# Kernel tuning notes

Measured on AMD Instinct MI355X. Metric: run time of the kernel, lower is better.

The kernel has to match this reference:

```python
import jax, jax.numpy as jnp
import numpy as np

EPS = 1e-5

def setup_inputs() -> dict:
    key = jax.random.key(0)
    ks = jax.random.split(key, 5)
    B, T, D = 2, 4096, 512
    x = jax.random.normal(ks[0], (B, T, D), dtype=jnp.float32)
    w_qkv = jax.random.normal(ks[1], (D, 3 * D), dtype=jnp.float32) * (1.0 / np.sqrt(D))
    w_out = jax.random.normal(ks[2], (D, D), dtype=jnp.float32) * (1.0 / np.sqrt(D))
    b_out = jnp.zeros((D,), dtype=jnp.float32)
    gamma = jnp.ones((D,), dtype=jnp.float32)
    beta = jnp.zeros((D,), dtype=jnp.float32)
    return {"x": x, "w_qkv": w_qkv, "w_out": w_out, "b_out": b_out,
            "gamma": gamma, "beta": beta}

def reference(x, w_qkv, w_out, b_out, gamma, beta):
    B, T, D = x.shape
    H = 8
    hd = D // H
    scale = 1.0 / jnp.sqrt(jnp.asarray(hd, x.dtype))
    residual = x
    # pre-norm LayerNorm
    mu = jnp.mean(x, axis=-1, keepdims=True)
    var = jnp.mean((x - mu) ** 2, axis=-1, keepdims=True)
    xn = (x - mu) / jnp.sqrt(var + EPS) * gamma + beta
    # qkv projection (no bias)
    qkv = (xn @ w_qkv).reshape(B, T, 3, H, hd)
    q, k, v = qkv[:, :, 0], qkv[:, :, 1], qkv[:, :, 2]  # (B,T,H,hd)
    # (B,H,T,T) scores with causal mask
    attn = jnp.einsum('bthd,bshd->bhts', q, k) * scale
    causal = jnp.triu(jnp.ones((T, T), dtype=bool), k=1)
    attn = jnp.where(causal[None, None], -jnp.inf, attn)
    attn = jax.nn.softmax(attn, axis=-1)
    out = jnp.einsum('bhts,bshd->bthd', attn, v).reshape(B, T, D)
    out = out @ w_out + b_out
    return out + residual
```

## Files before the change

### kernel.cpp

```cpp
#include <hip/hip_runtime.h>

typedef __attribute__((ext_vector_type(8))) short bh8;
typedef __attribute__((ext_vector_type(4))) float f32x4;
typedef unsigned short u16;

#define MFMA16 __builtin_amdgcn_mfma_f32_16x16x32_bf16

#if __has_builtin(__builtin_amdgcn_exp2f)
#define EXP2(x) __builtin_amdgcn_exp2f(x)
#else
#define EXP2(x) exp2f(x)
#endif

#define CEXP 0.18033688011112042f
#define MBIAS (10.0f * CEXP)

__device__ __forceinline__ u16 f2bf(float f) {
  union { float f; unsigned u; } v; v.f = f;
  unsigned r = v.u + 0x7fffu + ((v.u >> 16) & 1u);
  return (u16)(r >> 16);
}

__device__ __forceinline__ unsigned cvtpk(float lo, float hi) {
  unsigned r;
  asm("v_cvt_pk_bf16_f32 %0, %1, %2" : "=v"(r) : "v"(lo), "v"(hi));
  return r;
}

__device__ __forceinline__ void gload16(void* lds, const void* g) {
  __builtin_amdgcn_global_load_lds(
      (const __attribute__((address_space(1))) unsigned int*)g,
      (__attribute__((address_space(3))) unsigned int*)lds, 16, 0, 0);
}

__global__ __launch_bounds__(256) void k_ln(const float* __restrict__ x,
                                            const float* __restrict__ gamma,
                                            const float* __restrict__ beta,
                                            u16* __restrict__ xn) {
  int row  = blockIdx.x * 4 + (threadIdx.x >> 6);
  int lane = threadIdx.x & 63;
  const float4* xr = (const float4*)(x + row * 512);
  float4 a = xr[lane * 2], b = xr[lane * 2 + 1];
  float s  = a.x + a.y + a.z + a.w + b.x + b.y + b.z + b.w;
  float ss = a.x*a.x + a.y*a.y + a.z*a.z + a.w*a.w
           + b.x*b.x + b.y*b.y + b.z*b.z + b.w*b.w;
#pragma unroll
  for (int m = 1; m < 64; m <<= 1) { s += __shfl_xor(s, m, 64); ss += __shfl_xor(ss, m, 64); }
  float mu  = s * (1.0f / 512.0f);
  float var = ss * (1.0f / 512.0f) - mu * mu;
  float rstd = rsqrtf(var + 1e-5f);
  const float4* g4 = (const float4*)gamma;
  const float4* b4 = (const float4*)beta;
  float4 g0 = g4[lane * 2], g1 = g4[lane * 2 + 1];
  float4 e0 = b4[lane * 2], e1 = b4[lane * 2 + 1];
  bh8 ov;
  ov[0] = (short)f2bf((a.x - mu) * rstd * g0.x + e0.x);
  ov[1] = (short)f2bf((a.y - mu) * rstd * g0.y + e0.y);
  ov[2] = (short)f2bf((a.z - mu) * rstd * g0.z + e0.z);
  ov[3] = (short)f2bf((a.w - mu) * rstd * g0.w + e0.w);
  ov[4] = (short)f2bf((b.x - mu) * rstd * g1.x + e1.x);
  ov[5] = (short)f2bf((b.y - mu) * rstd * g1.y + e1.y);
  ov[6] = (short)f2bf((b.z - mu) * rstd * g1.z + e1.z);
  ov[7] = (short)f2bf((b.w - mu) * rstd * g1.w + e1.w);
  *(bh8*)(xn + row * 512 + lane * 8) = ov;
}

__global__ __launch_bounds__(256) void k_transpose_cast(const float* __restrict__ in,
                                                        u16* __restrict__ out,
                                                        int R, int C) {
  __shared__ float tile[32][33];
  int c0 = blockIdx.x * 32, r0 = blockIdx.y * 32;
  int tx = threadIdx.x & 31, ty = threadIdx.x >> 5;
#pragma unroll
  for (int i = 0; i < 32; i += 8)
    tile[ty + i][tx] = in[(r0 + ty + i) * C + (c0 + tx)];
  __syncthreads();
#pragma unroll
  for (int i = 0; i < 32; i += 8)
    out[(c0 + ty + i) * R + (r0 + tx)] = f2bf(tile[tx][ty + i]);
}

template <int EPI>
__global__ __launch_bounds__(256) void k_gemm(const u16* __restrict__ A,
                                              const u16* __restrict__ Bt,
                                              int N,
                                              u16* __restrict__ q, u16* __restrict__ kk, u16* __restrict__ vt,
                                              const float* __restrict__ bias,
                                              const float* __restrict__ resid,
                                              float* __restrict__ outp) {
  constexpr int K = 512, BM = 128, BK = 64;
  __shared__ u16 Al[BM * BK];
  __shared__ u16 Bl[BM * BK];
  int nBN = N / 128;
  int bid = (blockIdx.x & 7) * (gridDim.x >> 3) + (blockIdx.x >> 3);
  int m0 = (bid / nBN) * BM;
  int n0 = (bid % nBN) * 128;
  int tid = threadIdx.x, lane = tid & 63, w = tid >> 6;
  int l16 = lane & 15, lh = lane >> 4;
  int wm = (w >> 1) * 64, wn = (w & 1) * 64;
  const u16* Ab = A + m0 * K;
  const u16* Bb = Bt + n0 * K;
  f32x4 acc[4][4];
#pragma unroll
  for (int i = 0; i < 4; ++i)
#pragma unroll
    for (int j = 0; j < 4; ++j) acc[i][j] = (f32x4){0.f, 0.f, 0.f, 0.f};
  int srow = tid >> 3, schunk = tid & 7;
  for (int k0 = 0; k0 < K; k0 += BK) {
    __syncthreads();
#pragma unroll
    for (int j = 0; j < 4; ++j) {
      int r = j * 32 + srow;
      int sc = ((schunk ^ (r & 7)) << 3);
      gload16((char*)Al + j * 4096 + tid * 16, Ab + r * K + k0 + sc);
      gload16((char*)Bl + j * 4096 + tid * 16, Bb + r * K + k0 + sc);
    }
    __syncthreads();
#pragma unroll
    for (int c = 0; c < 2; ++c) {
      bh8 af[4], bf[4];
#pragma unroll
      for (int i = 0; i < 4; ++i) {
        int ra = wm + i * 16 + l16;
        af[i] = *(const bh8*)&Al[ra * 64 + ((c * 32 + lh * 8) ^ ((ra & 7) << 3))];
        int rb = wn + i * 16 + l16;
        bf[i] = *(const bh8*)&Bl[rb * 64 + ((c * 32 + lh * 8) ^ ((rb & 7) << 3))];
      }
#pragma unroll
      for (int mi = 0; mi < 4; ++mi)
#pragma unroll
        for (int ni = 0; ni < 4; ++ni)
          acc[mi][ni] = MFMA16(af[mi], bf[ni], acc[mi][ni], 0, 0, 0);
    }
  }
  if (EPI == 0) {
#pragma unroll
    for (int mi = 0; mi < 4; ++mi)
#pragma unroll
      for (int ni = 0; ni < 4; ++ni) {
        int col = n0 + wn + ni * 16 + l16;
        int s = col >> 9, h = (col >> 6) & 7, d = col & 63;
        int row0 = m0 + wm + mi * 16 + lh * 4;
        int b = row0 >> 12, t0 = row0 & 4095;
        if (s == 2) {
          uint2 pk;
          pk.x = cvtpk(acc[mi][ni][0], acc[mi][ni][1]);
          pk.y = cvtpk(acc[mi][ni][2], acc[mi][ni][3]);
          *(uint2*)&vt[((size_t)((b << 3) + h) * 64 + d) * 4096 + t0] = pk;
        } else {
          u16* base = (s == 0 ? q : kk);
#pragma unroll
          for (int j = 0; j < 4; ++j)
            base[(((size_t)(b << 3) + h) * 4096 + t0 + j) * 64 + d] = f2bf(acc[mi][ni][j]);
        }
      }
  } else {
#pragma unroll
    for (int mi = 0; mi < 4; ++mi)
#pragma unroll
      for (int ni = 0; ni < 4; ++ni) {
        int col = n0 + wn + ni * 16 + l16;
        float bo = bias[col];
#pragma unroll
        for (int j = 0; j < 4; ++j) {
          int row = m0 + wm + mi * 16 + lh * 4 + j;
          outp[row * 512 + col] = acc[mi][ni][j] + bo + resid[row * 512 + col];
        }
      }
  }
}

__global__ __launch_bounds__(256) void k_attn(const u16* __restrict__ Q,
                                              const u16* __restrict__ Kg,
                                              const u16* __restrict__ Vt,
                                              u16* __restrict__ O) {
  __shared__ u16 Kl[2 * 64 * 64];
  __shared__ u16 Vl[2 * 64 * 64];
  __shared__ u16 Pl[4 * 1024];
  int bh = blockIdx.x & 15;
  int qi = 63 - (blockIdx.x >> 4);
  int tid = threadIdx.x, lane = tid & 63, w = tid >> 6;
  int l16 = lane & 15, lh = lane >> 4;
  const u16* Qb = Q + bh * 4096 * 64;
  const u16* Kb = Kg + bh * 4096 * 64;
  const u16* Vb = Vt + (size_t)bh * 64 * 4096;
  int q0 = qi * 64;
  int myq = q0 + w * 16 + l16;
  bh8 qf0 = *(const bh8*)(Qb + myq * 64 + lh * 8);
  bh8 qf1 = *(const bh8*)(Qb + myq * 64 + 32 + lh * 8);
  float l_ = 0.f;
  f32x4 acc[4];
#pragma unroll
  for (int dn = 0; dn < 4; ++dn) acc[dn] = (f32x4){0.f, 0.f, 0.f, 0.f};
  int srow = tid >> 3, schunk = tid & 7;
  u16* pw = Pl + w * 1024 + l16 * 64;
  int pswz = (l16 & 7) << 3;

  for (int kt = 0; kt <= qi; kt += 2) {
    __syncthreads();
#pragma unroll
    for (int t = 0; t < 2; ++t) {
      int kk = (kt + t) * 64;
#pragma unroll
      for (int j = 0; j < 2; ++j) {
        int r = j * 32 + srow;
        int sc = ((schunk ^ (r & 7)) << 3);
        gload16((char*)Kl + t * 8192 + j * 4096 + tid * 16, Kb + (kk + r) * 64 + sc);
        gload16((char*)Vl + t * 8192 + j * 4096 + tid * 16, Vb + r * 4096 + kk + sc);
      }
    }
    __syncthreads();
    int k0 = kt * 64;
    f32x4 s[8];
    __builtin_amdgcn_s_setprio(1);
#pragma unroll
    for (int g = 0; g < 8; ++g) {
      const u16* Kc = Kl + (g >> 2) * 4096;
      int r = (g & 3) * 16 + l16;
      bh8 kf0 = *(const bh8*)&Kc[r * 64 + ((lh * 8) ^ ((r & 7) << 3))];
      bh8 kf1 = *(const bh8*)&Kc[r * 64 + ((32 + lh * 8) ^ ((r & 7) << 3))];
      f32x4 z = (f32x4){0.f, 0.f, 0.f, 0.f};
      z = MFMA16(kf0, qf0, z, 0, 0, 0);
      z = MFMA16(kf1, qf1, z, 0, 0, 0);
      s[g] = z;
    }
    __builtin_amdgcn_s_setprio(0);
    if (kt + 2 > qi) {
#pragma unroll
      for (int g = 0; g < 8; ++g)
#pragma unroll
        for (int j = 0; j < 4; ++j) {
          int tk = k0 + g * 16 + lh * 4 + j;
          if (tk > myq) s[g][j] = -3e38f;
        }
    }
#pragma unroll
    for (int g = 0; g < 8; ++g) {
      float p0 = EXP2(fmaf(s[g][0], CEXP, -MBIAS));
      float p1 = EXP2(fmaf(s[g][1], CEXP, -MBIAS));
      float p2 = EXP2(fmaf(s[g][2], CEXP, -MBIAS));
      float p3 = EXP2(fmaf(s[g][3], CEXP, -MBIAS));
      l_ += (p0 + p1) + (p2 + p3);
      s[g][0] = p0; s[g][1] = p1; s[g][2] = p2; s[g][3] = p3;
    }
#pragma unroll
    for (int h = 0; h < 2; ++h) {
#pragma unroll
      for (int f = 0; f < 4; ++f) {
        int g = h * 4 + f;
        uint2 pk;
        pk.x = cvtpk(s[g][0], s[g][1]);
        pk.y = cvtpk(s[g][2], s[g][3]);
        *(uint2*)&pw[(f * 16 + lh * 4) ^ pswz] = pk;
      }
      bh8 pa0 = *(const bh8*)&pw[(lh * 8) ^ pswz];
      bh8 pa1 = *(const bh8*)&pw[(32 + lh * 8) ^ pswz];
      const u16* Vc = Vl + h * 4096;
      __builtin_amdgcn_s_setprio(1);
#pragma unroll
      for (int dn = 0; dn < 4; ++dn) {
        int r = dn * 16 + l16;
        const u16* vr = Vc + r * 64;
        bh8 vb0 = *(const bh8*)&vr[(lh * 8) ^ ((r & 7) << 3)];
        bh8 vb1 = *(const bh8*)&vr[(32 + lh * 8) ^ ((r & 7) << 3)];
        acc[dn] = MFMA16(pa0, vb0, acc[dn], 0, 0, 0);
        acc[dn] = MFMA16(pa1, vb1, acc[dn], 0, 0, 0);
      }
      __builtin_amdgcn_s_setprio(0);
    }
  }
  l_ += __shfl_xor(l_, 16, 64);
  l_ += __shfl_xor(l_, 32, 64);
  float inv = 1.0f / l_;
  float i0 = __shfl(inv, lh * 4 + 0, 64);
  float i1 = __shfl(inv, lh * 4 + 1, 64);
  float i2 = __shfl(inv, lh * 4 + 2, 64);
  float i3 = __shfl(inv, lh * 4 + 3, 64);
  int b = bh >> 3, h = bh & 7;
#pragma unroll
  for (int j = 0; j < 4; ++j) {
    float iv = (j == 0 ? i0 : j == 1 ? i1 : j == 2 ? i2 : i3);
    int t = q0 + w * 16 + lh * 4 + j;
#pragma unroll
    for (int dn = 0; dn < 4; ++dn)
      O[(b * 4096 + t) * 512 + h * 64 + dn * 16 + l16] = f2bf(acc[dn][j] * iv);
  }
}

extern "C" void kernel_launch(void* const* d_in, const int* in_sizes, int n_in,
                              void* d_out, int out_size, void* d_ws, size_t ws_size,
                              hipStream_t stream) {
  const float* x     = (const float*)d_in[0];
  const float* w_qkv = (const float*)d_in[1];
  const float* w_out = (const float*)d_in[2];
  const float* b_out = (const float*)d_in[3];
  const float* gamma = (const float*)d_in[4];
  const float* beta  = (const float*)d_in[5];
  float* out = (float*)d_out;
  char* ws = (char*)d_ws;
  u16* xn    = (u16*)(ws);
  u16* wqkvT = (u16*)(ws + 8388608);
  u16* woutT = (u16*)(ws + 9961472);
  u16* q     = (u16*)(ws + 10485760);
  u16* k     = (u16*)(ws + 18874368);
  u16* vt    = (u16*)(ws + 27262976);
  u16* attn_out = xn;

  k_ln<<<2048, 256, 0, stream>>>(x, gamma, beta, xn);
  k_transpose_cast<<<dim3(48, 16), 256, 0, stream>>>(w_qkv, wqkvT, 512, 1536);
  k_transpose_cast<<<dim3(16, 16), 256, 0, stream>>>(w_out, woutT, 512, 512);
  k_gemm<0><<<64 * 12, 256, 0, stream>>>(xn, wqkvT, 1536, q, k, vt, nullptr, nullptr, nullptr);
  k_attn<<<1024, 256, 0, stream>>>(q, k, vt, attn_out);
  k_gemm<1><<<64 * 4, 256, 0, stream>>>(attn_out, woutT, 512, nullptr, nullptr, nullptr, b_out, x, out);
}
```

Baseline: 115.5 us.

## Switch attention kernel to 32x32x16 MFMA with key-split warps and LDS reduction

New measurement: 122.6 us. +6.1%, slower.

```diff
diff --git a/kernel.cpp b/kernel.cpp
--- a/kernel.cpp
+++ b/kernel.cpp
@@ -2,9 +2,11 @@
 
 typedef __attribute__((ext_vector_type(8))) short bh8;
 typedef __attribute__((ext_vector_type(4))) float f32x4;
+typedef __attribute__((ext_vector_type(16))) float f32x16;
 typedef unsigned short u16;
 
 #define MFMA16 __builtin_amdgcn_mfma_f32_16x16x32_bf16
+#define MFMA32 __builtin_amdgcn_mfma_f32_32x32x16_bf16
 
 #if __has_builtin(__builtin_amdgcn_exp2f)
 #define EXP2(x) __builtin_amdgcn_exp2f(x)
@@ -180,110 +182,132 @@
   int bh = blockIdx.x & 15;
   int qi = 63 - (blockIdx.x >> 4);
   int tid = threadIdx.x, lane = tid & 63, w = tid >> 6;
-  int l16 = lane & 15, lh = lane >> 4;
+  int l31 = lane & 31, hi = lane >> 5;
+  int qh = w >> 1, th = w & 1;
   const u16* Qb = Q + bh * 4096 * 64;
   const u16* Kb = Kg + bh * 4096 * 64;
   const u16* Vb = Vt + (size_t)bh * 64 * 4096;
   int q0 = qi * 64;
-  int myq = q0 + w * 16 + l16;
-  bh8 qf0 = *(const bh8*)(Qb + myq * 64 + lh * 8);
-  bh8 qf1 = *(const bh8*)(Qb + myq * 64 + 32 + lh * 8);
+  int myq = q0 + qh * 32 + l31;
+  bh8 qf[4];
+#pragma unroll
+  for (int ks = 0; ks < 4; ++ks)
+    qf[ks] = *(const bh8*)(Qb + myq * 64 + ks * 16 + hi * 8);
   float l_ = 0.f;
-  f32x4 acc[4];
-#pragma unroll
-  for (int dn = 0; dn < 4; ++dn) acc[dn] = (f32x4){0.f, 0.f, 0.f, 0.f};
+  f32x16 acc[2];
+#pragma unroll
+  for (int dh = 0; dh < 2; ++dh)
+#pragma unroll
+    for (int r = 0; r < 16; ++r) acc[dh][r] = 0.f;
   int srow = tid >> 3, schunk = tid & 7;
-  u16* pw = Pl + w * 1024 + l16 * 64;
-  int pswz = (l16 & 7) << 3;
+  u16* Pw = Pl + w * 1024;
+  int psw = (l31 & 3) << 1;
 
   for (int kt = 0; kt <= qi; kt += 2) {
     __syncthreads();
 #pragma unroll
     for (int t = 0; t < 2; ++t) {
-      int kk = (kt + t) * 64;
+      int kb = (kt + t) * 64;
 #pragma unroll
       for (int j = 0; j < 2; ++j) {
         int r = j * 32 + srow;
         int sc = ((schunk ^ (r & 7)) << 3);
-        gload16((char*)Kl + t * 8192 + j * 4096 + tid * 16, Kb + (kk + r) * 64 + sc);
-        gload16((char*)Vl + t * 8192 + j * 4096 + tid * 16, Vb + r * 4096 + kk + sc);
+        gload16((char*)Kl + t * 8192 + j * 4096 + tid * 16, Kb + (kb + r) * 64 + sc);
+        gload16((char*)Vl + t * 8192 + j * 4096 + tid * 16, Vb + r * 4096 + kb + sc);
       }
     }
     __syncthreads();
-    int k0 = kt * 64;
-    f32x4 s[8];
-    __builtin_amdgcn_s_setprio(1);
-#pragma unroll
-    for (int g = 0; g < 8; ++g) {
-      const u16* Kc = Kl + (g >> 2) * 4096;
-      int r = (g & 3) * 16 + l16;
-      bh8 kf0 = *(const bh8*)&Kc[r * 64 + ((lh * 8) ^ ((r & 7) << 3))];
-      bh8 kf1 = *(const bh8*)&Kc[r * 64 + ((32 + lh * 8) ^ ((r & 7) << 3))];
-      f32x4 z = (f32x4){0.f, 0.f, 0.f, 0.f};
-      z = MFMA16(kf0, qf0, z, 0, 0, 0);
-      z = MFMA16(kf1, qf1, z, 0, 0, 0);
-      s[g] = z;
-    }
-    __builtin_amdgcn_s_setprio(0);
-    if (kt + 2 > qi) {
-#pragma unroll
-      for (int g = 0; g < 8; ++g)
-#pragma unroll
-        for (int j = 0; j < 4; ++j) {
-          int tk = k0 + g * 16 + lh * 4 + j;
-          if (tk > myq) s[g][j] = -3e38f;
-        }
-    }
-#pragma unroll
-    for (int g = 0; g < 8; ++g) {
-      float p0 = EXP2(fmaf(s[g][0], CEXP, -MBIAS));
-      float p1 = EXP2(fmaf(s[g][1], CEXP, -MBIAS));
-      float p2 = EXP2(fmaf(s[g][2], CEXP, -MBIAS));
-      float p3 = EXP2(fmaf(s[g][3], CEXP, -MBIAS));
-      l_ += (p0 + p1) + (p2 + p3);
-      s[g][0] = p0; s[g][1] = p1; s[g][2] = p2; s[g][3] = p3;
-    }
-#pragma unroll
-    for (int h = 0; h < 2; ++h) {
-#pragma unroll
-      for (int f = 0; f < 4; ++f) {
-        int g = h * 4 + f;
+#pragma unroll
+    for (int t = 0; t < 2; ++t) {
+      int kz = kt + t;
+      const u16* Kc = Kl + t * 4096;
+      const u16* Vc = Vl + t * 4096;
+      f32x16 sa;
+#pragma unroll
+      for (int r = 0; r < 16; ++r) sa[r] = 0.f;
+      int rk = th * 32 + l31;
+      __builtin_amdgcn_s_setprio(1);
+#pragma unroll
+      for (int ks = 0; ks < 4; ++ks) {
+        int ck = ks * 2 + hi;
+        bh8 kf = *(const bh8*)&Kc[rk * 64 + ((ck ^ (rk & 7)) << 3)];
+        sa = MFMA32(kf, qf[ks], sa, 0, 0, 0);
+      }
+      __builtin_amdgcn_s_setprio(0);
+      if (kt + 2 > qi) {
+#pragma unroll
+        for (int r = 0; r < 16; ++r) {
+          int tkg = kz * 64 + th * 32 + (r & 3) + 8 * (r >> 2) + 4 * hi;
+          if (tkg > myq) sa[r] = -3e38f;
+        }
+      }
+      float p[16];
+#pragma unroll
+      for (int r = 0; r < 16; ++r) {
+        p[r] = EXP2(fmaf(sa[r], CEXP, -MBIAS));
+        l_ += p[r];
+      }
+#pragma unroll
+      for (int quad = 0; quad < 4; ++quad) {
         uint2 pk;
-        pk.x = cvtpk(s[g][0], s[g][1]);
-        pk.y = cvtpk(s[g][2], s[g][3]);
-        *(uint2*)&pw[(f * 16 + lh * 4) ^ pswz] = pk;
-      }
-      bh8 pa0 = *(const bh8*)&pw[(lh * 8) ^ pswz];
-      bh8 pa1 = *(const bh8*)&pw[(32 + lh * 8) ^ pswz];
-      const u16* Vc = Vl + h * 4096;
+        pk.x = cvtpk(p[quad * 4 + 0], p[quad * 4 + 1]);
+        pk.y = cvtpk(p[quad * 4 + 2], p[quad * 4 + 3]);
+        int s0 = quad * 2 + hi;
+        *(uint2*)&Pw[l31 * 32 + (((s0 ^ psw)) << 2)] = pk;
+      }
       __builtin_amdgcn_s_setprio(1);
 #pragma unroll
-      for (int dn = 0; dn < 4; ++dn) {
-        int r = dn * 16 + l16;
-        const u16* vr = Vc + r * 64;
-        bh8 vb0 = *(const bh8*)&vr[(lh * 8) ^ ((r & 7) << 3)];
-        bh8 vb1 = *(const bh8*)&vr[(32 + lh * 8) ^ ((r & 7) << 3)];
-        acc[dn] = MFMA16(pa0, vb0, acc[dn], 0, 0, 0);
-        acc[dn] = MFMA16(pa1, vb1, acc[dn], 0, 0, 0);
+      for (int dh = 0; dh < 2; ++dh) {
+        int rv = dh * 32 + l31;
+#pragma unroll
+        for (int k2 = 0; k2 < 2; ++k2) {
+          int sb = k2 * 4 + hi * 2;
+          bh8 pa = *(const bh8*)&Pw[l31 * 32 + ((sb ^ psw) << 2)];
+          int cv = th * 4 + k2 * 2 + hi;
+          bh8 vb = *(const bh8*)&Vc[rv * 64 + ((cv ^ (rv & 7)) << 3)];
+          acc[dh] = MFMA32(pa, vb, acc[dh], 0, 0, 0);
+        }
       }
       __builtin_amdgcn_s_setprio(0);
     }
   }
-  l_ += __shfl_xor(l_, 16, 64);
+  __syncthreads();
+  float* Ow = (float*)Kl;
+  float* Lw = (float*)Vl;
+  float* Iw = (float*)Vl + 128;
   l_ += __shfl_xor(l_, 32, 64);
-  float inv = 1.0f / l_;
-  float i0 = __shfl(inv, lh * 4 + 0, 64);
-  float i1 = __shfl(inv, lh * 4 + 1, 64);
-  float i2 = __shfl(inv, lh * 4 + 2, 64);
-  float i3 = __shfl(inv, lh * 4 + 3, 64);
-  int b = bh >> 3, h = bh & 7;
-#pragma unroll
-  for (int j = 0; j < 4; ++j) {
-    float iv = (j == 0 ? i0 : j == 1 ? i1 : j == 2 ? i2 : i3);
-    int t = q0 + w * 16 + lh * 4 + j;
-#pragma unroll
-    for (int dn = 0; dn < 4; ++dn)
-      O[(b * 4096 + t) * 512 + h * 64 + dn * 16 + l16] = f2bf(acc[dn][j] * iv);
+  if (hi == 0) Lw[(qh * 2 + th) * 32 + l31] = l_;
+  if (th == 0) {
+#pragma unroll
+    for (int dh = 0; dh < 2; ++dh)
+#pragma unroll
+      for (int r = 0; r < 16; ++r) {
+        int row = (r & 3) + 8 * (r >> 2) + 4 * hi;
+        Ow[qh * 2048 + row * 64 + dh * 32 + l31] = acc[dh][r];
+      }
+  }
+  __syncthreads();
+  float lt = Lw[(qh * 2) * 32 + l31] + Lw[(qh * 2 + 1) * 32 + l31];
+  float invq = 1.0f / lt;
+  if (hi == 0) Iw[qh * 32 + l31] = invq;
+  __syncthreads();
+  if (th == 1) {
+    int b = bh >> 3, h = bh & 7;
+#pragma unroll
+    for (int quad = 0; quad < 4; ++quad) {
+      f32x4 iv = *(const f32x4*)&Iw[qh * 32 + quad * 8 + hi * 4];
+#pragma unroll
+      for (int j = 0; j < 4; ++j) {
+        int r = quad * 4 + j;
+        int row = j + 8 * quad + 4 * hi;
+        int tg = q0 + qh * 32 + row;
+#pragma unroll
+        for (int dh = 0; dh < 2; ++dh) {
+          float o = acc[dh][r] + Ow[qh * 2048 + row * 64 + dh * 32 + l31];
+          O[((size_t)b * 4096 + tg) * 512 + h * 64 + dh * 32 + l31] = f2bf(o * iv[j]);
+        }
+      }
+    }
   }
 }
 
```
